# Optimization experiments

Measured on AMD Instinct MI355X. Metric: run time of the kernel, lower is better.

Reference implementation:

```python
import jax, jax.numpy as jnp
import numpy as np

T, B, D, H, HH, OUT = 512, 128, 256, 1024, 256, 128
EPS = 1e-3

def _ln(x, gamma, beta):
    # layer_norm over feature dim, eps=0.001, matching torch reciprocal(sqrt(var+eps))
    m = jnp.mean(x, -1, keepdims=True)
    xs = x - m
    v = jnp.mean(xs * xs, -1, keepdims=True)
    return gamma * xs * jax.lax.rsqrt(v + EPS) + beta

def _ln_all(h, base, units, gamma, beta):
    # normalize each of `base` gate blocks independently over `units`
    b = h.shape[0]
    hr = h.reshape(b, base, units)
    m = jnp.mean(hr, -1, keepdims=True)
    xs = hr - m
    v = jnp.mean(xs * xs, -1, keepdims=True)
    hn = (xs * jax.lax.rsqrt(v + EPS)).reshape(b, base * units)
    return gamma * hn + beta

def setup_inputs() -> dict:
    key = jax.random.key(0)
    ks = jax.random.split(key, 12)
    return {
        "x": jax.random.normal(ks[0], (T, B, D), jnp.float32),
        "Wx": jax.random.normal(ks[1], (4 * H, D), jnp.float32) * (1.0 / np.sqrt(D)),
        "Wh": jax.random.normal(ks[2], (4 * H, H), jnp.float32) * (1.0 / np.sqrt(H)),
        "bias": jax.random.normal(ks[3], (4 * H,), jnp.float32) * 0.1,
        "lna_gamma": jnp.ones((4 * H,), jnp.float32),
        "lna_beta": jnp.zeros((4 * H,), jnp.float32),
        "ln_gamma": jnp.ones((H,), jnp.float32),
        "ln_beta": jnp.zeros((H,), jnp.float32),
        "zb": jax.random.normal(ks[4], (4, HH, HH), jnp.float32) * 0.01,   # ib/jb/fb/ob _zb
        "zbeta": jax.random.normal(ks[5], (4, HH, H), jnp.float32) * 0.01, # ib/jb/fb/ob _beta
        "zw_w": jax.random.normal(ks[6], (8, HH, HH), jnp.float32) * 0.01, # ix,jx,fx,ox,ih,jh,fh,oh _zw_w
        "zw_b": jnp.ones((8, HH), jnp.float32),
        "alpha": jnp.full((8, HH, H), 0.1 / HH, jnp.float32) + jax.random.normal(ks[7], (8, HH, H), jnp.float32) * 1e-4,
        "hyp_Wx": jax.random.normal(ks[8], (4 * HH, D + H), jnp.float32) * (1.0 / np.sqrt(D + H)),
        "hyp_bx": jnp.zeros((4 * HH,), jnp.float32),
        "hyp_Wh": jax.random.normal(ks[9], (4 * HH, HH), jnp.float32) * (1.0 / np.sqrt(HH)),
        "hyp_bh": jnp.zeros((4 * HH,), jnp.float32),
        "hyp_lna_gamma": jnp.ones((4 * HH,), jnp.float32),
        "hyp_lna_beta": jnp.zeros((4 * HH,), jnp.float32),
        "hyp_ln_gamma": jnp.ones((HH,), jnp.float32),
        "hyp_ln_beta": jnp.zeros((HH,), jnp.float32),
        "fc_W": jax.random.normal(ks[10], (OUT, H), jnp.float32) * (1.0 / np.sqrt(H)),
        "fc_b": jnp.zeros((OUT,), jnp.float32),
    }

def reference(x, Wx, Wh, bias, lna_gamma, lna_beta, ln_gamma, ln_beta, zb, zbeta,
              zw_w, zw_b, alpha, hyp_Wx, hyp_bx, hyp_Wh, hyp_bh,
              hyp_lna_gamma, hyp_lna_beta, hyp_ln_gamma, hyp_ln_beta, fc_W, fc_b):
    b4 = bias.reshape(4, H)

    def step(carry, xt):
        h, c, hh, ch = carry  # main (B,H), hyper (B,HH)
        # ---- hypernetwork LSTM cell (layer-norm LSTM) ----
        g = jnp.concatenate([xt, h], 1) @ hyp_Wx.T + hyp_bx + hh @ hyp_Wh.T + hyp_bh
        g = _ln_all(g, 4, HH, hyp_lna_gamma, hyp_lna_beta)
        hi, hf, hg, ho = jnp.split(g, 4, 1)  # ingate, forgetgate, cellgate, outgate
        ch_n = jax.nn.sigmoid(hf) * ch + jax.nn.sigmoid(hi) * jnp.tanh(hg)
        hyp = jax.nn.sigmoid(ho) * jnp.tanh(_ln(ch_n, hyp_ln_gamma, hyp_ln_beta))
        # ---- hyper-modulation: per-gate scale vectors and bias adjustments ----
        z = jnp.einsum('bq,kqp->kbp', hyp, zw_w) + zw_b[:, None, :]   # (8,B,HH)
        sc = jnp.einsum('kbp,kph->kbh', z, alpha)                     # (8,B,H)
        bz = jnp.einsum('bq,kqp->kbp', hyp, zb)                       # (4,B,HH)
        badj = jnp.einsum('kbp,kph->kbh', bz, zbeta)                  # (4,B,H)
        # ---- main LSTM gates (order i, j, f, o) ----
        xg = (xt @ Wx.T).reshape(B, 4, H).transpose(1, 0, 2)          # (4,B,H)
        hg2 = (h @ Wh.T).reshape(B, 4, H).transpose(1, 0, 2)          # (4,B,H)
        gates = sc[:4] * xg + sc[4:] * hg2 + b4[:, None, :] + badj    # (4,B,H)
        gates = _ln_all(gates.transpose(1, 0, 2).reshape(B, 4 * H), 4, H, lna_gamma, lna_beta)
        i, j, f, o = jnp.split(gates, 4, 1)
        c_n = jax.nn.sigmoid(f) * c + jax.nn.sigmoid(i) * jnp.tanh(j)
        h_n = jax.nn.sigmoid(o) * jnp.tanh(_ln(c_n, ln_gamma, ln_beta))
        return (h_n, c_n, hyp, ch_n), None

    init = (jnp.zeros((B, H), x.dtype), jnp.zeros((B, H), x.dtype),
            jnp.zeros((B, HH), x.dtype), jnp.zeros((B, HH), x.dtype))
    (h_f, _, _, _), _ = jax.lax.scan(step, init, x)
    return h_f @ fc_W.T + fc_b  # (B, OUT)
```

## Files before the change

kernel.cpp:

```cpp
#include <hip/hip_runtime.h>
#include <math.h>

#define T_STEPS 512
#define BATCH   128
#define DIN     256
#define HMAIN   1024
#define HHYP    256
#define OUTN    128
#define EPS     1e-3f

#define KSPLIT_NONE (1<<30)

typedef __attribute__((ext_vector_type(4))) float f32x4;
typedef __attribute__((ext_vector_type(8))) short s16x8;

__device__ __forceinline__ float sigm(float x){ return 1.f/(1.f + expf(-x)); }

__device__ __forceinline__ unsigned short f2bf(float f){
    union { float f; unsigned u; } x; x.f = f;
    unsigned r = x.u + 0x7FFFu + ((x.u >> 16) & 1u);
    return (unsigned short)(r >> 16);
}

#define BM 32
#define BN 64
#define KT 32
__device__ void gemm_dev(const float* __restrict__ A1, int lda1, int ksplit,
                         const float* __restrict__ A2, int lda2,
                         const float* __restrict__ Bp, int ldb, int b_nk,
                         const float* __restrict__ bias,
                         float* __restrict__ C, int ldc,
                         int K, int k0, int mtile, int ntile)
{
    __shared__ __align__(16) float As[KT][BM+4];
    __shared__ __align__(16) float Bs[KT][BN+4];
    const int tid = threadIdx.x;
    const int mt = tid >> 4, nt = tid & 15;
    const int m0g = mtile*BM, n0g = ntile*BN;
    float acc[4][4];
    #pragma unroll
    for (int i=0;i<4;++i) { acc[i][0]=0;acc[i][1]=0;acc[i][2]=0;acc[i][3]=0; }
    for (int kt = 0; kt < K; kt += KT) {
        __syncthreads();
        #pragma unroll
        for (int i=0;i<8;++i){
            int e = tid + i*128;
            int m = e >> 5, k = e & 31;
            int gk = k0 + kt + k, gm = m0g + m;
            float v = (gk < ksplit) ? A1[(size_t)gm*lda1 + gk]
                                    : A2[(size_t)gm*lda2 + (gk - ksplit)];
            As[k][m] = v;
        }
        if (b_nk) {
            #pragma unroll
            for (int i=0;i<16;++i){
                int e = tid + i*128;
                int n = e >> 5, k = e & 31;
                Bs[k][n] = Bp[(size_t)(n0g + n)*ldb + (k0 + kt + k)];
            }
        } else {
            #pragma unroll
            for (int i=0;i<16;++i){
                int e = tid + i*128;
                int k = e >> 6, n = e & 63;
                Bs[k][n] = Bp[(size_t)(k0 + kt + k)*ldb + (n0g + n)];
            }
        }
        __syncthreads();
        #pragma unroll
        for (int k=0;k<KT;++k){
            float4 av = *(const float4*)(&As[k][4*mt]);
            float4 bv = *(const float4*)(&Bs[k][4*nt]);
            acc[0][0]+=av.x*bv.x; acc[0][1]+=av.x*bv.y; acc[0][2]+=av.x*bv.z; acc[0][3]+=av.x*bv.w;
            acc[1][0]+=av.y*bv.x; acc[1][1]+=av.y*bv.y; acc[1][2]+=av.y*bv.z; acc[1][3]+=av.y*bv.w;
            acc[2][0]+=av.z*bv.x; acc[2][1]+=av.z*bv.y; acc[2][2]+=av.z*bv.z; acc[2][3]+=av.z*bv.w;
            acc[3][0]+=av.w*bv.x; acc[3][1]+=av.w*bv.y; acc[3][2]+=av.w*bv.z; acc[3][3]+=av.w*bv.w;
        }
    }
    #pragma unroll
    for (int i=0;i<4;++i){
        int gm = m0g + 4*mt + i;
        #pragma unroll
        for (int j=0;j<4;++j){
            int gn = n0g + 4*nt + j;
            float v = acc[i][j];
            if (bias) v += bias[gn];
            C[(size_t)gm*ldc + gn] = v;
        }
    }
}

#define ASTR 40
__device__ void gemm_mfma(const float* __restrict__ A1, int lda1, int ksplit,
                          const float* __restrict__ A2, int lda2,
                          const unsigned short* __restrict__ B, int ldb,
                          const float* __restrict__ bias,
                          float* __restrict__ C, int ldc,
                          int K, int k0, int mtile, int ntile)
{
    __shared__ __align__(16) unsigned short As[32*ASTR];
    __shared__ __align__(16) unsigned short Bs[128*ASTR];
    const int tid = threadIdx.x;
    const int lane = tid & 63, w = tid >> 6;
    const int wm = (w >> 1) * 16, wn = (w & 1) * 64;
    const int fr = lane & 15, koff = (lane >> 4) * 8;
    const int m0g = mtile*32, n0g = ntile*128;

    f32x4 acc[4];
    #pragma unroll
    for (int j=0;j<4;++j) acc[j] = (f32x4){0.f,0.f,0.f,0.f};

    const int arow = tid >> 3, akc = (tid & 7) * 4;
    for (int kt = 0; kt < K; kt += 32) {
        __syncthreads();
        {
            int gk = k0 + kt + akc;
            int gm = m0g + arow;
            const float* src = (gk < ksplit) ? (A1 + (size_t)gm*lda1 + gk)
                                             : (A2 + (size_t)gm*lda2 + (gk - ksplit));
            float4 v = *(const float4*)src;
            unsigned short* d = &As[arow*ASTR + akc];
            d[0] = f2bf(v.x); d[1] = f2bf(v.y); d[2] = f2bf(v.z); d[3] = f2bf(v.w);
        }
        #pragma unroll
        for (int i=0;i<4;++i){
            int e = tid + i*256;
            int n = e >> 3, kc = (e & 7) * 4;
            ushort4 bv = *(const ushort4*)(B + (size_t)(n0g + n)*ldb + (k0 + kt + kc));
            unsigned short* d = &Bs[n*ASTR + kc];
            d[0] = bv.x; d[1] = bv.y; d[2] = bv.z; d[3] = bv.w;
        }
        __syncthreads();
        s16x8 af = *(const s16x8*)&As[(wm + fr)*ASTR + koff];
        #pragma unroll
        for (int j=0;j<4;++j){
            s16x8 bf = *(const s16x8*)&Bs[(wn + j*16 + fr)*ASTR + koff];
            acc[j] = __builtin_amdgcn_mfma_f32_16x16x32_bf16(af, bf, acc[j], 0, 0, 0);
        }
    }
    #pragma unroll
    for (int j=0;j<4;++j){
        int gn = n0g + wn + j*16 + fr;
        float bb = bias ? bias[gn] : 0.f;
        #pragma unroll
        for (int r=0;r<4;++r){
            int gm = m0g + wm + (lane >> 4)*4 + r;
            C[(size_t)gm*ldc + gn] = acc[j][r] + bb;
        }
    }
}

__global__ __launch_bounds__(256) void k_prep_convert(
    const float* __restrict__ hyp_Wx, const float* __restrict__ hyp_Wh,
    const float* __restrict__ hyp_bx, const float* __restrict__ hyp_bh,
    const float* __restrict__ Wx, const float* __restrict__ Wh,
    unsigned short* __restrict__ wcat1bf, unsigned short* __restrict__ wxbf,
    unsigned short* __restrict__ whbf, float* __restrict__ bias1,
    float* __restrict__ act1, float* __restrict__ c, float* __restrict__ ch)
{
    size_t i = (size_t)blockIdx.x*256 + threadIdx.x;
    if (i < 1572864u) {
        int n = (int)(i / 1536), k = (int)(i % 1536);
        float v = (k < 1280) ? hyp_Wx[(size_t)n*1280 + k] : hyp_Wh[(size_t)n*256 + (k-1280)];
        wcat1bf[i] = f2bf(v); return;
    }
    i -= 1572864u;
    if (i < 1048576u) { wxbf[i] = f2bf(Wx[i]); return; }
    i -= 1048576u;
    if (i < 4194304u) { whbf[i] = f2bf(Wh[i]); return; }
    i -= 4194304u;
    if (i < 1024u) { bias1[i] = hyp_bx[i] + hyp_bh[i]; return; }
    i -= 1024u;
    if (i < 163840u) { act1[i] = 0.f; return; }
    i -= 163840u;
    if (i < 131072u) { c[i] = 0.f; return; }
    i -= 131072u;
    if (i < 32768u) { ch[i] = 0.f; return; }
}

__global__ __launch_bounds__(128) void k_prep_wcomb(
    const float* __restrict__ zw_w, const float* __restrict__ zb,
    const float* __restrict__ alpha, const float* __restrict__ zbeta,
    float* __restrict__ wcombf32)
{
    int kk = blockIdx.z;
    const float* A = (kk < 8) ? (zw_w + (size_t)kk*65536) : (zb + (size_t)(kk-8)*65536);
    const float* Bm = (kk < 8) ? (alpha + (size_t)kk*262144) : (zbeta + (size_t)(kk-8)*262144);
    gemm_dev(A, 256, KSPLIT_NONE, A, 256, Bm, 1024, 0, nullptr,
             wcombf32 + (size_t)kk*262144, 1024, 256, 0, blockIdx.x, blockIdx.y);
}

__global__ __launch_bounds__(256) void k_prep_cvtcomb(
    const float* __restrict__ wcombf32, unsigned short* __restrict__ wcombbf)
{
    size_t i = (size_t)blockIdx.x*256 + threadIdx.x;
    if (i >= 3145728u) return;
    int kk = (int)(i / 262144u);
    int r  = (int)(i % 262144u);
    int n = r / 256, k = r % 256;
    wcombbf[i] = f2bf(wcombf32[(size_t)kk*262144 + (size_t)k*1024 + n]);
}

__global__ __launch_bounds__(256) void k_prep_bcomb(
    const float* __restrict__ zw_b, const float* __restrict__ alpha,
    float* __restrict__ bcomb)
{
    int k = blockIdx.x;
    int n = blockIdx.y*256 + threadIdx.x;
    float s = 0.f;
    for (int p=0;p<256;++p)
        s += zw_b[k*256+p] * alpha[(size_t)k*262144 + (size_t)p*1024 + n];
    bcomb[(size_t)k*1024 + n] = s;
}

__global__ __launch_bounds__(256) void k_step1(
    const float* __restrict__ xt, const float* __restrict__ act1,
    const unsigned short* __restrict__ wcat1bf,
    const unsigned short* __restrict__ wxbf, const unsigned short* __restrict__ whbf,
    float* __restrict__ gpart, float* __restrict__ xghg)
{
    int bid = blockIdx.x;
    if (bid < 128) {
        int sp = bid >> 5, r = bid & 31;
        gemm_mfma(xt, 256, 256, act1, 1280, wcat1bf, 1536, nullptr,
                  gpart + (size_t)sp*131072, 1024, 384, sp*384, r >> 3, r & 7);
    } else if (bid < 256) {
        int r = bid - 128;
        gemm_mfma(xt, 256, KSPLIT_NONE, xt, 256, wxbf, 256, nullptr,
                  xghg, 4096, 256, 0, r >> 5, r & 31);
    } else {
        int r = bid - 256;
        gemm_mfma(act1, 1280, KSPLIT_NONE, act1, 1280, whbf, 1024, nullptr,
                  xghg + 524288, 4096, 1024, 0, r >> 5, r & 31);
    }
}

__global__ __launch_bounds__(256) void k_step2(
    const float* __restrict__ act1, const unsigned short* __restrict__ wcombbf,
    const float* __restrict__ bcomb, float* __restrict__ scb)
{
    int bid = blockIdx.x;
    int kk = bid >> 5, r = bid & 31;
    const float* bias = (kk < 8) ? (bcomb + (size_t)kk*1024) : nullptr;
    gemm_mfma(act1 + 1024, 1280, KSPLIT_NONE, act1 + 1024, 1280,
              wcombbf + (size_t)kk*262144, 256, bias,
              scb + (size_t)kk*131072, 1024, 256, 0, r >> 3, r & 7);
}

__device__ __forceinline__ void breduce2(float& a, float& b, volatile float* buf, int tid){
    #pragma unroll
    for (int off = 32; off > 0; off >>= 1) { a += __shfl_xor(a, off); b += __shfl_xor(b, off); }
    __syncthreads();
    if ((tid & 63) == 0) { buf[(tid>>6)*2] = a; buf[(tid>>6)*2+1] = b; }
    __syncthreads();
    a = buf[0] + buf[2] + buf[4] + buf[6];
    b = buf[1] + buf[3] + buf[5] + buf[7];
}

__global__ __launch_bounds__(256) void k_hyper_cell(
    const float* __restrict__ lna_g, const float* __restrict__ lna_b,
    const float* __restrict__ ln_g, const float* __restrict__ ln_b,
    const float* __restrict__ gpart, const float* __restrict__ bias1,
    float* __restrict__ ch, float* __restrict__ act1)
{
    __shared__ float buf[8];
    int b = blockIdx.x, tid = threadIdx.x;
    float v[4];
    #pragma unroll
    for (int g=0; g<4; ++g){
        int idx = b*1024 + g*256 + tid;
        v[g] = gpart[idx] + gpart[131072 + idx] + gpart[262144 + idx] + gpart[393216 + idx]
             + bias1[g*256 + tid];
    }
    #pragma unroll
    for (int g=0; g<4; ++g){
        float s = v[g], ss = v[g]*v[g];
        breduce2(s, ss, buf, tid);
        float m = s * (1.f/256.f);
        float var = ss * (1.f/256.f) - m*m;
        v[g] = (v[g]-m)*rsqrtf(var + EPS)*lna_g[g*256+tid] + lna_b[g*256+tid];
    }
    float chp = ch[b*256 + tid];
    float cn = sigm(v[1])*chp + sigm(v[0])*tanhf(v[2]);
    float s = cn, ss = cn*cn;
    breduce2(s, ss, buf, tid);
    float m = s*(1.f/256.f);
    float var = ss*(1.f/256.f) - m*m;
    float hn = sigm(v[3]) * tanhf((cn-m)*rsqrtf(var + EPS)*ln_g[tid] + ln_b[tid]);
    ch[b*256 + tid] = cn;
    act1[b*1280 + 1024 + tid] = hn;
}

__global__ __launch_bounds__(256) void k_main_cell(
    const float* __restrict__ bias4,
    const float* __restrict__ lna_g, const float* __restrict__ lna_b,
    const float* __restrict__ ln_g, const float* __restrict__ ln_b,
    const float* __restrict__ xghg, const float* __restrict__ scb,
    float* __restrict__ c, float* __restrict__ act1)
{
    __shared__ float buf[8];
    int b = blockIdx.x, tid = threadIdx.x;
    float gn[4][4];
    #pragma unroll
    for (int k=0;k<4;++k){
        float pre[4]; float s=0.f, ss=0.f;
        #pragma unroll
        for (int j=0;j<4;++j){
            int h = j*256 + tid;
            int n = k*1024 + h;
            int bh = b*1024 + h;
            float xgv = xghg[b*4096 + n];
            float hgv = xghg[524288 + b*4096 + n];
            float p = scb[k*131072 + bh]*xgv + scb[(4+k)*131072 + bh]*hgv
                    + bias4[n] + scb[(8+k)*131072 + bh];
            pre[j] = p; s += p; ss += p*p;
        }
        breduce2(s, ss, buf, tid);
        float m = s*(1.f/1024.f);
        float var = ss*(1.f/1024.f) - m*m;
        float rs = rsqrtf(var + EPS);
        #pragma unroll
        for (int j=0;j<4;++j){
            int h=j*256+tid, n=k*1024+h;
            gn[k][j] = (pre[j]-m)*rs*lna_g[n] + lna_b[n];
        }
    }
    float cnv[4]; float s=0.f, ss=0.f;
    #pragma unroll
    for (int j=0;j<4;++j){
        int h=j*256+tid;
        float cv = c[b*1024+h];
        float x = sigm(gn[2][j])*cv + sigm(gn[0][j])*tanhf(gn[1][j]);
        cnv[j]=x; s+=x; ss+=x*x;
    }
    breduce2(s, ss, buf, tid);
    float m=s*(1.f/1024.f);
    float var=ss*(1.f/1024.f)-m*m;
    float rs=rsqrtf(var + EPS);
    #pragma unroll
    for (int j=0;j<4;++j){
        int h=j*256+tid;
        float hv = sigm(gn[3][j])*tanhf((cnv[j]-m)*rs*ln_g[h] + ln_b[h]);
        c[b*1024+h] = cnv[j];
        act1[b*1280 + h] = hv;
    }
}

__global__ __launch_bounds__(128) void k_fc(
    const float* __restrict__ fcW, const float* __restrict__ fcb,
    const float* __restrict__ act1, float* __restrict__ out)
{
    int b = blockIdx.x, o = threadIdx.x;
    const float* h = act1 + (size_t)b*1280;
    float s = fcb[o];
    for (int k=0;k<1024;++k) s += h[k]*fcW[(size_t)o*1024 + k];
    out[b*OUTN + o] = s;
}

extern "C" void kernel_launch(void* const* d_in, const int* in_sizes, int n_in,
                              void* d_out, int out_size, void* d_ws, size_t ws_size,
                              hipStream_t stream)
{
    const float* x        = (const float*)d_in[0];
    const float* Wx       = (const float*)d_in[1];
    const float* Wh       = (const float*)d_in[2];
    const float* bias     = (const float*)d_in[3];
    const float* lna_g    = (const float*)d_in[4];
    const float* lna_b    = (const float*)d_in[5];
    const float* ln_g     = (const float*)d_in[6];
    const float* ln_b     = (const float*)d_in[7];
    const float* zb       = (const float*)d_in[8];
    const float* zbeta    = (const float*)d_in[9];
    const float* zw_w     = (const float*)d_in[10];
    const float* zw_b     = (const float*)d_in[11];
    const float* alpha    = (const float*)d_in[12];
    const float* hyp_Wx   = (const float*)d_in[13];
    const float* hyp_bx   = (const float*)d_in[14];
    const float* hyp_Wh   = (const float*)d_in[15];
    const float* hyp_bh   = (const float*)d_in[16];
    const float* hlna_g   = (const float*)d_in[17];
    const float* hlna_b   = (const float*)d_in[18];
    const float* hln_g    = (const float*)d_in[19];
    const float* hln_b    = (const float*)d_in[20];
    const float* fcW      = (const float*)d_in[21];
    const float* fcb      = (const float*)d_in[22];
    float* out = (float*)d_out;

    unsigned short* wcat1bf = (unsigned short*)d_ws;
    unsigned short* wxbf    = wcat1bf + 1572864;
    unsigned short* whbf    = wxbf + 1048576;
    unsigned short* wcombbf = whbf + 4194304;
    float* bcomb = (float*)(wcombbf + 3145728);
    float* bias1 = bcomb + 8192;
    float* act1  = bias1 + 1024;
    float* c     = act1 + 163840;
    float* ch    = c + 131072;
    float* stepbuf = ch + 32768;
    float* gpart = stepbuf;
    float* scb   = gpart + 524288;
    float* xghg  = scb + 1572864;
    float* wcombf32 = stepbuf;

    k_prep_convert<<<(7144448 + 255)/256, 256, 0, stream>>>(
        hyp_Wx, hyp_Wh, hyp_bx, hyp_bh, Wx, Wh,
        wcat1bf, wxbf, whbf, bias1, act1, c, ch);
    k_prep_wcomb<<<dim3(8,16,12), 128, 0, stream>>>(zw_w, zb, alpha, zbeta, wcombf32);
    k_prep_bcomb<<<dim3(8,4), 256, 0, stream>>>(zw_b, alpha, bcomb);
    k_prep_cvtcomb<<<(3145728 + 255)/256, 256, 0, stream>>>(wcombf32, wcombbf);

    for (int t = 0; t < T_STEPS; ++t) {
        const float* xt = x + (size_t)t*BATCH*DIN;
        k_step1<<<384, 256, 0, stream>>>(xt, act1, wcat1bf, wxbf, whbf, gpart, xghg);
        k_hyper_cell<<<BATCH, 256, 0, stream>>>(hlna_g, hlna_b, hln_g, hln_b,
                                                gpart, bias1, ch, act1);
        k_step2<<<384, 256, 0, stream>>>(act1, wcombbf, bcomb, scb);
        k_main_cell<<<BATCH, 256, 0, stream>>>(bias, lna_g, lna_b, ln_g, ln_b,
                                               xghg, scb, c, act1);
    }

    k_fc<<<BATCH, 128, 0, stream>>>(fcW, fcb, act1, out);
}
```

Baseline: 34.19 ms.

## Replace per-step kernel launches with a persistent cooperative kernel using grid sync

```diff
diff --git a/kernel.cpp b/kernel.cpp
--- a/kernel.cpp
+++ b/kernel.cpp
@@ -1,5 +1,8 @@
 #include <hip/hip_runtime.h>
+#include <hip/hip_cooperative_groups.h>
 #include <math.h>
+
+namespace cg = cooperative_groups;
 
 #define T_STEPS 512
 #define BATCH   128
@@ -213,40 +216,6 @@
     bcomb[(size_t)k*1024 + n] = s;
 }
 
-__global__ __launch_bounds__(256) void k_step1(
-    const float* __restrict__ xt, const float* __restrict__ act1,
-    const unsigned short* __restrict__ wcat1bf,
-    const unsigned short* __restrict__ wxbf, const unsigned short* __restrict__ whbf,
-    float* __restrict__ gpart, float* __restrict__ xghg)
-{
-    int bid = blockIdx.x;
-    if (bid < 128) {
-        int sp = bid >> 5, r = bid & 31;
-        gemm_mfma(xt, 256, 256, act1, 1280, wcat1bf, 1536, nullptr,
-                  gpart + (size_t)sp*131072, 1024, 384, sp*384, r >> 3, r & 7);
-    } else if (bid < 256) {
-        int r = bid - 128;
-        gemm_mfma(xt, 256, KSPLIT_NONE, xt, 256, wxbf, 256, nullptr,
-                  xghg, 4096, 256, 0, r >> 5, r & 31);
-    } else {
-        int r = bid - 256;
-        gemm_mfma(act1, 1280, KSPLIT_NONE, act1, 1280, whbf, 1024, nullptr,
-                  xghg + 524288, 4096, 1024, 0, r >> 5, r & 31);
-    }
-}
-
-__global__ __launch_bounds__(256) void k_step2(
-    const float* __restrict__ act1, const unsigned short* __restrict__ wcombbf,
-    const float* __restrict__ bcomb, float* __restrict__ scb)
-{
-    int bid = blockIdx.x;
-    int kk = bid >> 5, r = bid & 31;
-    const float* bias = (kk < 8) ? (bcomb + (size_t)kk*1024) : nullptr;
-    gemm_mfma(act1 + 1024, 1280, KSPLIT_NONE, act1 + 1024, 1280,
-              wcombbf + (size_t)kk*262144, 256, bias,
-              scb + (size_t)kk*131072, 1024, 256, 0, r >> 3, r & 7);
-}
-
 __device__ __forceinline__ void breduce2(float& a, float& b, volatile float* buf, int tid){
     #pragma unroll
     for (int off = 32; off > 0; off >>= 1) { a += __shfl_xor(a, off); b += __shfl_xor(b, off); }
@@ -257,20 +226,27 @@
     b = buf[1] + buf[3] + buf[5] + buf[7];
 }
 
-__global__ __launch_bounds__(256) void k_hyper_cell(
-    const float* __restrict__ lna_g, const float* __restrict__ lna_b,
-    const float* __restrict__ ln_g, const float* __restrict__ ln_b,
-    const float* __restrict__ gpart, const float* __restrict__ bias1,
-    float* __restrict__ ch, float* __restrict__ act1)
+struct Params {
+    const float *x;
+    const float *bias4, *lna_g, *lna_b, *ln_g, *ln_b;
+    const float *hlna_g, *hlna_b, *hln_g, *hln_b;
+    const float *fcW, *fcb;
+    const unsigned short *wcat1bf, *wxbf, *whbf, *wcombbf;
+    const float *bcomb, *bias1;
+    float *act1, *c, *ch, *gpart, *scb, *xghg;
+    float *out;
+};
+
+__device__ void hyper_cell_dev(int b, const Params& p)
 {
     __shared__ float buf[8];
-    int b = blockIdx.x, tid = threadIdx.x;
+    int tid = threadIdx.x;
     float v[4];
     #pragma unroll
     for (int g=0; g<4; ++g){
         int idx = b*1024 + g*256 + tid;
-        v[g] = gpart[idx] + gpart[131072 + idx] + gpart[262144 + idx] + gpart[393216 + idx]
-             + bias1[g*256 + tid];
+        v[g] = p.gpart[idx] + p.gpart[131072 + idx] + p.gpart[262144 + idx] + p.gpart[393216 + idx]
+             + p.bias1[g*256 + tid];
     }
     #pragma unroll
     for (int g=0; g<4; ++g){
@@ -278,28 +254,23 @@
         breduce2(s, ss, buf, tid);
         float m = s * (1.f/256.f);
         float var = ss * (1.f/256.f) - m*m;
-        v[g] = (v[g]-m)*rsqrtf(var + EPS)*lna_g[g*256+tid] + lna_b[g*256+tid];
-    }
-    float chp = ch[b*256 + tid];
+        v[g] = (v[g]-m)*rsqrtf(var + EPS)*p.hlna_g[g*256+tid] + p.hlna_b[g*256+tid];
+    }
+    float chp = p.ch[b*256 + tid];
     float cn = sigm(v[1])*chp + sigm(v[0])*tanhf(v[2]);
     float s = cn, ss = cn*cn;
     breduce2(s, ss, buf, tid);
     float m = s*(1.f/256.f);
     float var = ss*(1.f/256.f) - m*m;
-    float hn = sigm(v[3]) * tanhf((cn-m)*rsqrtf(var + EPS)*ln_g[tid] + ln_b[tid]);
-    ch[b*256 + tid] = cn;
-    act1[b*1280 + 1024 + tid] = hn;
-}
-
-__global__ __launch_bounds__(256) void k_main_cell(
-    const float* __restrict__ bias4,
-    const float* __restrict__ lna_g, const float* __restrict__ lna_b,
-    const float* __restrict__ ln_g, const float* __restrict__ ln_b,
-    const float* __restrict__ xghg, const float* __restrict__ scb,
-    float* __restrict__ c, float* __restrict__ act1)
+    float hn = sigm(v[3]) * tanhf((cn-m)*rsqrtf(var + EPS)*p.hln_g[tid] + p.hln_b[tid]);
+    p.ch[b*256 + tid] = cn;
+    p.act1[b*1280 + 1024 + tid] = hn;
+}
+
+__device__ void main_cell_dev(int b, const Params& p)
 {
     __shared__ float buf[8];
-    int b = blockIdx.x, tid = threadIdx.x;
+    int tid = threadIdx.x;
     float gn[4][4];
     #pragma unroll
     for (int k=0;k<4;++k){
@@ -309,11 +280,11 @@
             int h = j*256 + tid;
             int n = k*1024 + h;
             int bh = b*1024 + h;
-            float xgv = xghg[b*4096 + n];
-            float hgv = xghg[524288 + b*4096 + n];
-            float p = scb[k*131072 + bh]*xgv + scb[(4+k)*131072 + bh]*hgv
-                    + bias4[n] + scb[(8+k)*131072 + bh];
-            pre[j] = p; s += p; ss += p*p;
+            float xgv = p.xghg[b*4096 + n];
+            float hgv = p.xghg[524288 + b*4096 + n];
+            float pr = p.scb[k*131072 + bh]*xgv + p.scb[(4+k)*131072 + bh]*hgv
+                     + p.bias4[n] + p.scb[(8+k)*131072 + bh];
+            pre[j] = pr; s += pr; ss += pr*pr;
         }
         breduce2(s, ss, buf, tid);
         float m = s*(1.f/1024.f);
@@ -322,16 +293,16 @@
         #pragma unroll
         for (int j=0;j<4;++j){
             int h=j*256+tid, n=k*1024+h;
-            gn[k][j] = (pre[j]-m)*rs*lna_g[n] + lna_b[n];
+            gn[k][j] = (pre[j]-m)*rs*p.lna_g[n] + p.lna_b[n];
         }
     }
     float cnv[4]; float s=0.f, ss=0.f;
     #pragma unroll
     for (int j=0;j<4;++j){
         int h=j*256+tid;
-        float cv = c[b*1024+h];
-        float x = sigm(gn[2][j])*cv + sigm(gn[0][j])*tanhf(gn[1][j]);
-        cnv[j]=x; s+=x; ss+=x*x;
+        float cv = p.c[b*1024+h];
+        float xv = sigm(gn[2][j])*cv + sigm(gn[0][j])*tanhf(gn[1][j]);
+        cnv[j]=xv; s+=xv; ss+=xv*xv;
     }
     breduce2(s, ss, buf, tid);
     float m=s*(1.f/1024.f);
@@ -340,21 +311,62 @@
     #pragma unroll
     for (int j=0;j<4;++j){
         int h=j*256+tid;
-        float hv = sigm(gn[3][j])*tanhf((cnv[j]-m)*rs*ln_g[h] + ln_b[h]);
-        c[b*1024+h] = cnv[j];
-        act1[b*1280 + h] = hv;
-    }
-}
-
-__global__ __launch_bounds__(128) void k_fc(
-    const float* __restrict__ fcW, const float* __restrict__ fcb,
-    const float* __restrict__ act1, float* __restrict__ out)
-{
-    int b = blockIdx.x, o = threadIdx.x;
-    const float* h = act1 + (size_t)b*1280;
-    float s = fcb[o];
-    for (int k=0;k<1024;++k) s += h[k]*fcW[(size_t)o*1024 + k];
-    out[b*OUTN + o] = s;
+        float hv = sigm(gn[3][j])*tanhf((cnv[j]-m)*rs*p.ln_g[h] + p.ln_b[h]);
+        p.c[b*1024+h] = cnv[j];
+        p.act1[b*1280 + h] = hv;
+    }
+}
+
+__global__ __launch_bounds__(256, 2) void k_persist(Params p)
+{
+    cg::grid_group grid = cg::this_grid();
+    const int nb = gridDim.x, bid = blockIdx.x;
+
+    for (int t = 0; t < T_STEPS; ++t) {
+        const float* xt = p.x + (size_t)t*BATCH*DIN;
+
+        for (int job = bid; job < 384; job += nb) {
+            if (job < 128) {
+                int sp = job >> 5, r = job & 31;
+                gemm_mfma(xt, 256, 256, p.act1, 1280, p.wcat1bf, 1536, nullptr,
+                          p.gpart + (size_t)sp*131072, 1024, 384, sp*384, r >> 3, r & 7);
+            } else if (job < 256) {
+                int r = job - 128;
+                gemm_mfma(xt, 256, KSPLIT_NONE, xt, 256, p.wxbf, 256, nullptr,
+                          p.xghg, 4096, 256, 0, r >> 5, r & 31);
+            } else {
+                int r = job - 256;
+                gemm_mfma(p.act1, 1280, KSPLIT_NONE, p.act1, 1280, p.whbf, 1024, nullptr,
+                          p.xghg + 524288, 4096, 1024, 0, r >> 5, r & 31);
+            }
+        }
+        grid.sync();
+
+        for (int b = bid; b < 128; b += nb) hyper_cell_dev(b, p);
+        grid.sync();
+
+        for (int job = bid; job < 384; job += nb) {
+            int kk = job >> 5, r = job & 31;
+            const float* bias = (kk < 8) ? (p.bcomb + (size_t)kk*1024) : nullptr;
+            gemm_mfma(p.act1 + 1024, 1280, KSPLIT_NONE, p.act1 + 1024, 1280,
+                      p.wcombbf + (size_t)kk*262144, 256, bias,
+                      p.scb + (size_t)kk*131072, 1024, 256, 0, r >> 3, r & 7);
+        }
+        grid.sync();
+
+        for (int b = bid; b < 128; b += nb) main_cell_dev(b, p);
+        grid.sync();
+    }
+
+    for (int b = bid; b < 128; b += nb) {
+        int o = threadIdx.x;
+        if (o < OUTN) {
+            const float* h = p.act1 + (size_t)b*1280;
+            float s = p.fcb[o];
+            for (int k=0;k<1024;++k) s += h[k]*p.fcW[(size_t)o*1024 + k];
+            p.out[b*OUTN + o] = s;
+        }
+    }
 }
 
 extern "C" void kernel_launch(void* const* d_in, const int* in_sizes, int n_in,
@@ -384,7 +396,6 @@
     const float* hln_b    = (const float*)d_in[20];
     const float* fcW      = (const float*)d_in[21];
     const float* fcb      = (const float*)d_in[22];
-    float* out = (float*)d_out;
 
     unsigned short* wcat1bf = (unsigned short*)d_ws;
     unsigned short* wxbf    = wcat1bf + 1572864;
@@ -408,15 +419,24 @@
     k_prep_bcomb<<<dim3(8,4), 256, 0, stream>>>(zw_b, alpha, bcomb);
     k_prep_cvtcomb<<<(3145728 + 255)/256, 256, 0, stream>>>(wcombf32, wcombbf);
 
-    for (int t = 0; t < T_STEPS; ++t) {
-        const float* xt = x + (size_t)t*BATCH*DIN;
-        k_step1<<<384, 256, 0, stream>>>(xt, act1, wcat1bf, wxbf, whbf, gpart, xghg);
-        k_hyper_cell<<<BATCH, 256, 0, stream>>>(hlna_g, hlna_b, hln_g, hln_b,
-                                                gpart, bias1, ch, act1);
-        k_step2<<<384, 256, 0, stream>>>(act1, wcombbf, bcomb, scb);
-        k_main_cell<<<BATCH, 256, 0, stream>>>(bias, lna_g, lna_b, ln_g, ln_b,
-                                               xghg, scb, c, act1);
-    }
-
-    k_fc<<<BATCH, 128, 0, stream>>>(fcW, fcb, act1, out);
-}
+    Params p;
+    p.x = x; p.bias4 = bias;
+    p.lna_g = lna_g; p.lna_b = lna_b; p.ln_g = ln_g; p.ln_b = ln_b;
+    p.hlna_g = hlna_g; p.hlna_b = hlna_b; p.hln_g = hln_g; p.hln_b = hln_b;
+    p.fcW = fcW; p.fcb = fcb;
+    p.wcat1bf = wcat1bf; p.wxbf = wxbf; p.whbf = whbf; p.wcombbf = wcombbf;
+    p.bcomb = bcomb; p.bias1 = bias1;
+    p.act1 = act1; p.c = c; p.ch = ch;
+    p.gpart = gpart; p.scb = scb; p.xghg = xghg;
+    p.out = (float*)d_out;
+
+    int maxb = 0;
+    hipOccupancyMaxActiveBlocksPerMultiprocessor(&maxb, (const void*)k_persist, 256, 0);
+    if (maxb < 1) maxb = 1;
+    int grid = maxb * 256;
+    if (grid > 512) grid = 512;
+
+    void* args[] = { (void*)&p };
+    hipLaunchCooperativeKernel((const void*)k_persist, dim3(grid), dim3(256),
+                               args, 0, stream);
+}
```

Result: slower. 86.81 ms (+153.9%).
